# Kernel optimization log

Measured on AMD Instinct MI355X. Metric: run time of the kernel, lower is better.

## Reference

```python
import jax, jax.numpy as jnp
import numpy as np

N_QUBITS = 10
DEPTH = 4


def _cz_sign(n):
    # Diagonal of product of CZ(q, q+1) for q in 0..n-2 (qubit q = bit q, little-endian).
    idx = np.arange(2 ** n)
    bits = (idx[:, None] >> np.arange(n)) & 1            # (2^n, n)
    pairs = (bits[:, :-1] & bits[:, 1:]).sum(axis=1)
    return jnp.asarray(1 - 2 * (pairs & 1), jnp.float32)  # (2^n,)


def _z_matrix(n):
    # Column i = diagonal of Z on qubit n-1-i (Qiskit label 'I'*i + 'Z' + ...).
    idx = np.arange(2 ** n)
    bits = (idx[:, None] >> np.arange(n)) & 1
    return jnp.asarray((1 - 2 * bits)[:, ::-1], jnp.float32)  # (2^n, n)


def _quantum_features(x, theta):
    B, n = x.shape
    depth = theta.shape[0]
    half = 0.5 * x
    c = jnp.cos(half).astype(jnp.complex64)
    s = jnp.sin(half).astype(jnp.complex64)
    # Initial state: per-sample product of RX(x_q)|0> = [cos(x/2), -i sin(x/2)].
    # Build as kron over qubits, MSB (qubit n-1) first -> flat index bit q = qubit q.
    state = jnp.ones((B, 1), jnp.complex64)
    for q in reversed(range(n)):
        v = jnp.stack([c[:, q], -1j * s[:, q]], axis=-1)  # (B, 2)
        state = (state[:, :, None] * v[:, None, :]).reshape(B, -1)
    cz = _cz_sign(n)
    for l in range(depth):
        for q in range(n):
            th = 0.5 * theta[l, q]
            ct = jnp.cos(th).astype(jnp.complex64)
            st = jnp.sin(th).astype(jnp.complex64)
            gate = jnp.stack([jnp.stack([ct, -st]), jnp.stack([st, ct])])  # (2,2) RY
            left, right = 2 ** (n - 1 - q), 2 ** q
            state = jnp.einsum('ij,bljr->blir', gate,
                               state.reshape(B, left, 2, right)).reshape(B, -1)
        state = state * cz  # all CZ(q,q+1) at once (diagonal)
    probs = state.real ** 2 + state.imag ** 2          # (B, 2^n)
    return probs @ _z_matrix(n)                        # (B, n) <Z_i> expectations


def setup_inputs() -> dict:
    key = jax.random.key(0)
    ks = jax.random.split(key, 6)
    B, F, D = 4096, N_QUBITS, DEPTH
    x = jax.random.normal(ks[0], (B, F), jnp.float32)
    Ws = jax.random.normal(ks[1], (D + 1, F, F), jnp.float32) / np.sqrt(F).astype(np.float32)
    bs = 0.01 * jax.random.normal(ks[2], (D + 1, F), jnp.float32)
    theta = jax.random.normal(ks[3], (D, F), jnp.float32)
    W_final = jax.random.normal(ks[4], (2, 2 * F), jnp.float32) / np.sqrt(2 * F).astype(np.float32)
    b_final = 0.01 * jax.random.normal(ks[5], (2,), jnp.float32)
    return {"x": x, "Ws": Ws, "bs": bs, "theta": theta,
            "W_final": W_final, "b_final": b_final}


def reference(x, Ws, bs, theta, W_final, b_final):
    # Classical stack: depth x (Linear + ReLU) then a final Linear (same width).
    h = x
    for l in range(DEPTH):
        h = jax.nn.relu(h @ Ws[l].T + bs[l])
    cls_out = h @ Ws[DEPTH].T + bs[DEPTH]              # (B, F)
    qfeat = _quantum_features(x, theta)                # (B, n_qubits)
    combined = jnp.concatenate([cls_out, qfeat], axis=1)
    return combined @ W_final.T + b_final              # (B, 2) logits
```

## Files before the change

kernel.cpp:

```cpp
#include <hip/hip_runtime.h>
#include <math.h>

#define NQ 10
#define QDEPTH 4
#define BLK 256
#define WPS 4

typedef float v2f __attribute__((ext_vector_type(2)));

__device__ __forceinline__ int   asi(float v) { return __builtin_bit_cast(int, v); }
__device__ __forceinline__ float asf(int v)   { return __builtin_bit_cast(float, v); }

template<int D>
__device__ __forceinline__ float exch(float v, int addr32) {
    if constexpr (D == 1)
        return asf(__builtin_amdgcn_update_dpp(asi(v), asi(v), 0xB1, 0xF, 0xF, true));
    else if constexpr (D == 2)
        return asf(__builtin_amdgcn_update_dpp(asi(v), asi(v), 0x4E, 0xF, 0xF, true));
    else if constexpr (D == 4)
        return asf(__builtin_amdgcn_ds_swizzle(asi(v), 0x101F));
    else if constexpr (D == 8)
        return asf(__builtin_amdgcn_ds_swizzle(asi(v), 0x201F));
    else if constexpr (D == 16)
        return asf(__builtin_amdgcn_ds_swizzle(asi(v), 0x401F));
    else
        return asf(__builtin_amdgcn_ds_bpermute(addr32, asi(v)));
}

__device__ __forceinline__ float rlane(float v, int l) {
    return asf(__builtin_amdgcn_readlane(asi(v), l));
}

template<int Q>
__device__ __forceinline__ void local_gate_t(v2f (&P)[16], float t) {
    const v2f tt = {t, t};
    #pragma unroll
    for (int pp = 0; pp < 8; ++pp) {
        const int i0 = ((pp >> Q) << (Q + 1)) | (pp & ((1 << Q) - 1));
        const int i1 = i0 | (1 << Q);
        v2f a = P[i0], b = P[i1];
        P[i0] = a - tt * b;
        P[i1] = b + tt * a;
    }
}

template<int D>
__device__ __forceinline__ void cross_gate_t(v2f (&P)[16], float tvv, int addr32) {
    const v2f tt = {tvv, tvv};
    #pragma unroll
    for (int r = 0; r < 16; ++r) {
        v2f pp;
        pp.x = exch<D>(P[r].x, addr32);
        pp.y = exch<D>(P[r].y, addr32);
        P[r] = P[r] + tt * pp;
    }
}

__global__ __launch_bounds__(BLK, 4) void hybrid_kernel(
    const float* __restrict__ x,
    const float* __restrict__ Ws,
    const float* __restrict__ bs,
    const float* __restrict__ theta,
    const float* __restrict__ Wf,
    const float* __restrict__ bfin,
    float* __restrict__ out)
{
    const int tid  = threadIdx.x;
    const int lane = tid & 63;
    const int wv   = tid >> 6;
    const int s    = blockIdx.x * WPS + wv;

    float ang = 0.0f;
    if (lane < QDEPTH * NQ)              ang = theta[lane];
    else if (lane < QDEPTH * NQ + NQ)    ang = x[s * NQ + (lane - QDEPTH * NQ)];
    float sv_, cv_;
    sincosf(0.5f * ang, &sv_, &cv_);
    const float tv_ = sv_ / cv_;

    const int addr32 = (lane ^ 32) << 2;

    float cc = (lane < QDEPTH * NQ) ? cv_ : 1.0f;
    cc *= exch<1>(cc, addr32);
    cc *= exch<2>(cc, addr32);
    cc *= exch<4>(cc, addr32);
    cc *= exch<8>(cc, addr32);
    cc *= exch<16>(cc, addr32);
    cc *= exch<32>(cc, addr32);
    const float C2 = cc * cc;

    const int pl = __popc(lane);
    v2f P[16];
    {
        float cq[4], sq[4];
        #pragma unroll
        for (int q = 0; q < 4; ++q) {
            cq[q] = rlane(cv_, QDEPTH * NQ + q);
            sq[q] = rlane(sv_, QDEPTH * NQ + q);
        }
        float lf = 1.0f;
        #pragma unroll
        for (int b = 0; b < 6; ++b) {
            float cb = rlane(cv_, QDEPTH * NQ + 4 + b);
            float sb = rlane(sv_, QDEPTH * NQ + 4 + b);
            lf *= ((lane >> b) & 1) ? sb : cb;
        }
        float p01[4], p23[4];
        p01[0] = cq[0] * cq[1]; p01[1] = sq[0] * cq[1];
        p01[2] = cq[0] * sq[1]; p01[3] = sq[0] * sq[1];
        p23[0] = cq[2] * cq[3]; p23[1] = sq[2] * cq[3];
        p23[2] = cq[2] * sq[3]; p23[3] = sq[2] * sq[3];
        #pragma unroll
        for (int loc = 0; loc < 16; ++loc) {
            float r = lf * p01[loc & 3] * p23[loc >> 2];
            int pm = (pl + __popc(loc)) & 3;
            P[loc].x = (pm == 0) ? r : ((pm == 2) ? -r : 0.0f);
            P[loc].y = (pm == 1) ? -r : ((pm == 3) ? r : 0.0f);
        }
    }

    int zmask[6];
    #pragma unroll
    for (int b = 0; b < 6; ++b)
        zmask[b] = ((lane >> b) & 1) << 31;

    const int p3  = __popc(lane & (lane >> 1)) & 1;
    const int sAw = p3 << 31;
    const int sBw = (p3 ^ (lane & 1)) << 31;
    const int sAn = sAw ^ 0x80000000;
    const int sBn = sBw ^ 0x80000000;

    for (int l = 0; l < QDEPTH; ++l) {
        local_gate_t<0>(P, rlane(tv_, l * NQ + 0));
        local_gate_t<1>(P, rlane(tv_, l * NQ + 1));
        local_gate_t<2>(P, rlane(tv_, l * NQ + 2));
        local_gate_t<3>(P, rlane(tv_, l * NQ + 3));
        {
            float tvv;
            tvv = asf(asi(-rlane(tv_, l * NQ + 4)) ^ zmask[0]);
            cross_gate_t<1>(P, tvv, addr32);
            tvv = asf(asi(-rlane(tv_, l * NQ + 5)) ^ zmask[1]);
            cross_gate_t<2>(P, tvv, addr32);
            tvv = asf(asi(-rlane(tv_, l * NQ + 6)) ^ zmask[2]);
            cross_gate_t<4>(P, tvv, addr32);
            tvv = asf(asi(-rlane(tv_, l * NQ + 7)) ^ zmask[3]);
            cross_gate_t<8>(P, tvv, addr32);
            tvv = asf(asi(-rlane(tv_, l * NQ + 8)) ^ zmask[4]);
            cross_gate_t<16>(P, tvv, addr32);
            tvv = asf(asi(-rlane(tv_, l * NQ + 9)) ^ zmask[5]);
            cross_gate_t<32>(P, tvv, addr32);
        }
        #pragma unroll
        for (int loc = 0; loc < 16; ++loc) {
            const int C1 = __popc(loc & (loc >> 1)) & 1;
            const int m  = (loc & 8) ? (C1 ? sBn : sBw) : (C1 ? sAn : sAw);
            P[loc].x = asf(asi(P[loc].x) ^ m);
            P[loc].y = asf(asi(P[loc].y) ^ m);
        }
    }

    float pr[16], S = 0.0f;
    #pragma unroll
    for (int loc = 0; loc < 16; ++loc) {
        pr[loc] = fmaf(P[loc].x, P[loc].x, P[loc].y * P[loc].y);
        S += pr[loc];
    }
    float U0 = 0.0f, U1 = 0.0f, U2 = 0.0f, U3 = 0.0f;
    #pragma unroll
    for (int loc = 0; loc < 16; ++loc) {
        if (loc & 1) U0 += pr[loc];
        if (loc & 2) U1 += pr[loc];
        if (loc & 4) U2 += pr[loc];
        if (loc & 8) U3 += pr[loc];
    }
    const float w00 = Wf[19], w01 = Wf[18], w02 = Wf[17], w03 = Wf[16];
    const float w10 = Wf[39], w11 = Wf[38], w12 = Wf[37], w13 = Wf[36];
    float d0 = ((w00 + w01) + (w02 + w03)) * S;
    float d1 = ((w10 + w11) + (w12 + w13)) * S;
    d0 = fmaf(-2.0f * w00, U0, d0); d0 = fmaf(-2.0f * w01, U1, d0);
    d0 = fmaf(-2.0f * w02, U2, d0); d0 = fmaf(-2.0f * w03, U3, d0);
    d1 = fmaf(-2.0f * w10, U0, d1); d1 = fmaf(-2.0f * w11, U1, d1);
    d1 = fmaf(-2.0f * w12, U2, d1); d1 = fmaf(-2.0f * w13, U3, d1);
    float L0 = 0.0f, L1 = 0.0f;
    #pragma unroll
    for (int b = 0; b < 6; ++b) {
        L0 += asf(asi(Wf[15 - b]) ^ zmask[b]);
        L1 += asf(asi(Wf[35 - b]) ^ zmask[b]);
    }
    float qp0 = fmaf(L0, S, d0);
    float qp1 = fmaf(L1, S, d1);
    qp0 += exch<1>(qp0, addr32);  qp1 += exch<1>(qp1, addr32);
    qp0 += exch<2>(qp0, addr32);  qp1 += exch<2>(qp1, addr32);
    qp0 += exch<4>(qp0, addr32);  qp1 += exch<4>(qp1, addr32);
    qp0 += exch<8>(qp0, addr32);  qp1 += exch<8>(qp1, addr32);
    qp0 += exch<16>(qp0, addr32); qp1 += exch<16>(qp1, addr32);
    qp0 += exch<32>(qp0, addr32); qp1 += exch<32>(qp1, addr32);

    const int row = (lane < NQ) ? lane : 0;
    float h = x[s * NQ + row];
    #pragma unroll
    for (int l = 0; l < QDEPTH; ++l) {
        float v = bs[l * NQ + row];
        #pragma unroll
        for (int j = 0; j < NQ; ++j)
            v = fmaf(Ws[(l * NQ + row) * NQ + j], rlane(h, j), v);
        h = fmaxf(v, 0.0f);
    }
    float cls = bs[QDEPTH * NQ + row];
    #pragma unroll
    for (int j = 0; j < NQ; ++j)
        cls = fmaf(Ws[(QDEPTH * NQ + row) * NQ + j], rlane(h, j), cls);

    float o0 = fmaf(C2, qp0, bfin[0]);
    float o1 = fmaf(C2, qp1, bfin[1]);
    #pragma unroll
    for (int j = 0; j < NQ; ++j) {
        float cj = rlane(cls, j);
        o0 = fmaf(Wf[j],      cj, o0);
        o1 = fmaf(Wf[20 + j], cj, o1);
    }
    if (lane == 0) {
        float2 o; o.x = o0; o.y = o1;
        *reinterpret_cast<float2*>(&out[s * 2]) = o;
    }
}

extern "C" void kernel_launch(void* const* d_in, const int* in_sizes, int n_in,
                              void* d_out, int out_size, void* d_ws, size_t ws_size,
                              hipStream_t stream) {
    const float* x     = (const float*)d_in[0];
    const float* Ws    = (const float*)d_in[1];
    const float* bs    = (const float*)d_in[2];
    const float* theta = (const float*)d_in[3];
    const float* Wf    = (const float*)d_in[4];
    const float* bfin  = (const float*)d_in[5];
    float* out = (float*)d_out;

    const int B = in_sizes[0] / NQ;
    hybrid_kernel<<<B / WPS, BLK, 0, stream>>>(x, Ws, bs, theta, Wf, bfin, out);
}
```

Baseline: 24.79 us.

## Replace LDS-based lane exchanges with DPP and permlane swaps, fast sincos

Replaces the ds_swizzle/ds_bpermute exchanges for lane distances 8, 16 and 32 with a DPP row-shuffle and gfx950 permlane16/32 swap instructions. The 16- and 32-distance gates are reformulated around the pairwise sum the swap returns, so the partner value is never fetched directly. Also swaps sincosf for a custom range-reduced polynomial with a hardware reciprocal, and turns the CZ sign XOR into a multiply by ±1. This removes LDS-path latency from the cross-lane gates and reductions, at the cost of extra arithmetic and some rounding differences from the sum-based gate formula. The DPP control 0x128 for distance 8 is a row-rotate, and its correctness for a butterfly exchange is questionable.

```diff
diff --git a/kernel.cpp b/kernel.cpp
--- a/kernel.cpp
+++ b/kernel.cpp
@@ -12,23 +12,61 @@
 __device__ __forceinline__ float asf(int v)   { return __builtin_bit_cast(float, v); }
 
 template<int D>
-__device__ __forceinline__ float exch(float v, int addr32) {
+__device__ __forceinline__ float exch(float v) {
     if constexpr (D == 1)
         return asf(__builtin_amdgcn_update_dpp(asi(v), asi(v), 0xB1, 0xF, 0xF, true));
     else if constexpr (D == 2)
         return asf(__builtin_amdgcn_update_dpp(asi(v), asi(v), 0x4E, 0xF, 0xF, true));
-    else if constexpr (D == 4)
+    else if constexpr (D == 8)
+        return asf(__builtin_amdgcn_update_dpp(asi(v), asi(v), 0x128, 0xF, 0xF, true));
+    else
         return asf(__builtin_amdgcn_ds_swizzle(asi(v), 0x101F));
-    else if constexpr (D == 8)
-        return asf(__builtin_amdgcn_ds_swizzle(asi(v), 0x201F));
-    else if constexpr (D == 16)
-        return asf(__builtin_amdgcn_ds_swizzle(asi(v), 0x401F));
-    else
-        return asf(__builtin_amdgcn_ds_bpermute(addr32, asi(v)));
+}
+
+__device__ __forceinline__ float plsum16(float v) {
+    unsigned u = (unsigned)asi(v);
+    auto r = __builtin_amdgcn_permlane16_swap(u, u, false, false);
+    return asf((int)r[0]) + asf((int)r[1]);
+}
+__device__ __forceinline__ float plsum32(float v) {
+    unsigned u = (unsigned)asi(v);
+    auto r = __builtin_amdgcn_permlane32_swap(u, u, false, false);
+    return asf((int)r[0]) + asf((int)r[1]);
+}
+__device__ __forceinline__ float plmul16(float v) {
+    unsigned u = (unsigned)asi(v);
+    auto r = __builtin_amdgcn_permlane16_swap(u, u, false, false);
+    return asf((int)r[0]) * asf((int)r[1]);
+}
+__device__ __forceinline__ float plmul32(float v) {
+    unsigned u = (unsigned)asi(v);
+    auto r = __builtin_amdgcn_permlane32_swap(u, u, false, false);
+    return asf((int)r[0]) * asf((int)r[1]);
 }
 
 __device__ __forceinline__ float rlane(float v, int l) {
     return asf(__builtin_amdgcn_readlane(asi(v), l));
+}
+
+__device__ __forceinline__ void fast_sincos(float h, float* sp, float* cp) {
+    float nf = __builtin_rintf(h * 0.31830987f);
+    float r  = fmaf(nf, -3.14159274f, h);
+    r        = fmaf(nf,  8.7422777e-8f, r);
+    int  sg  = (((int)nf) & 1) << 31;
+    float x2 = r * r;
+    float q  = fmaf(x2, -2.5052108e-8f, 2.7557319e-6f);
+    q = fmaf(x2, q, -1.9841270e-4f);
+    q = fmaf(x2, q,  8.3333333e-3f);
+    q = fmaf(x2, q, -0.16666667f);
+    float s  = fmaf(r * x2, q, r);
+    float c2 = fmaf(x2,  2.0876757e-9f, -2.7557319e-7f);
+    c2 = fmaf(x2, c2,  2.4801587e-5f);
+    c2 = fmaf(x2, c2, -1.3888889e-3f);
+    c2 = fmaf(x2, c2,  4.1666667e-2f);
+    c2 = fmaf(x2, c2, -0.5f);
+    float c  = fmaf(x2, c2, 1.0f);
+    *sp = asf(asi(s) ^ sg);
+    *cp = asf(asi(c) ^ sg);
 }
 
 template<int Q>
@@ -45,14 +83,28 @@
 }
 
 template<int D>
-__device__ __forceinline__ void cross_gate_t(v2f (&P)[16], float tvv, int addr32) {
+__device__ __forceinline__ void cross_gate_t(v2f (&P)[16], float tvv) {
     const v2f tt = {tvv, tvv};
     #pragma unroll
     for (int r = 0; r < 16; ++r) {
         v2f pp;
-        pp.x = exch<D>(P[r].x, addr32);
-        pp.y = exch<D>(P[r].y, addr32);
+        pp.x = exch<D>(P[r].x);
+        pp.y = exch<D>(P[r].y);
         P[r] = P[r] + tt * pp;
+    }
+}
+
+template<int D>
+__device__ __forceinline__ void cross_gate_pl(v2f (&P)[16], float tvv) {
+    const v2f tt = {tvv, tvv};
+    const float om = 1.0f - tvv;
+    const v2f om2 = {om, om};
+    #pragma unroll
+    for (int r = 0; r < 16; ++r) {
+        v2f S;
+        if constexpr (D == 16) { S.x = plsum16(P[r].x); S.y = plsum16(P[r].y); }
+        else                   { S.x = plsum32(P[r].x); S.y = plsum32(P[r].y); }
+        P[r] = om2 * P[r] + tt * S;
     }
 }
 
@@ -74,18 +126,16 @@
     if (lane < QDEPTH * NQ)              ang = theta[lane];
     else if (lane < QDEPTH * NQ + NQ)    ang = x[s * NQ + (lane - QDEPTH * NQ)];
     float sv_, cv_;
-    sincosf(0.5f * ang, &sv_, &cv_);
-    const float tv_ = sv_ / cv_;
-
-    const int addr32 = (lane ^ 32) << 2;
+    fast_sincos(0.5f * ang, &sv_, &cv_);
+    const float tv_ = sv_ * __builtin_amdgcn_rcpf(cv_);
 
     float cc = (lane < QDEPTH * NQ) ? cv_ : 1.0f;
-    cc *= exch<1>(cc, addr32);
-    cc *= exch<2>(cc, addr32);
-    cc *= exch<4>(cc, addr32);
-    cc *= exch<8>(cc, addr32);
-    cc *= exch<16>(cc, addr32);
-    cc *= exch<32>(cc, addr32);
+    cc *= exch<1>(cc);
+    cc *= exch<2>(cc);
+    cc *= exch<4>(cc);
+    cc *= exch<8>(cc);
+    cc  = plmul16(cc);
+    cc  = plmul32(cc);
     const float C2 = cc * cc;
 
     const int pl = __popc(lane);
@@ -124,10 +174,10 @@
         zmask[b] = ((lane >> b) & 1) << 31;
 
     const int p3  = __popc(lane & (lane >> 1)) & 1;
-    const int sAw = p3 << 31;
-    const int sBw = (p3 ^ (lane & 1)) << 31;
-    const int sAn = sAw ^ 0x80000000;
-    const int sBn = sBw ^ 0x80000000;
+    const float sAf = asf(0x3F800000 ^ (p3 << 31));
+    const float sBf = asf(0x3F800000 ^ ((p3 ^ (lane & 1)) << 31));
+    const v2f sA2 = { sAf,  sAf}, sB2 = { sBf,  sBf};
+    const v2f nA2 = {-sAf, -sAf}, nB2 = {-sBf, -sBf};
 
     for (int l = 0; l < QDEPTH; ++l) {
         local_gate_t<0>(P, rlane(tv_, l * NQ + 0));
@@ -137,24 +187,23 @@
         {
             float tvv;
             tvv = asf(asi(-rlane(tv_, l * NQ + 4)) ^ zmask[0]);
-            cross_gate_t<1>(P, tvv, addr32);
+            cross_gate_t<1>(P, tvv);
             tvv = asf(asi(-rlane(tv_, l * NQ + 5)) ^ zmask[1]);
-            cross_gate_t<2>(P, tvv, addr32);
+            cross_gate_t<2>(P, tvv);
             tvv = asf(asi(-rlane(tv_, l * NQ + 6)) ^ zmask[2]);
-            cross_gate_t<4>(P, tvv, addr32);
+            cross_gate_t<4>(P, tvv);
             tvv = asf(asi(-rlane(tv_, l * NQ + 7)) ^ zmask[3]);
-            cross_gate_t<8>(P, tvv, addr32);
+            cross_gate_t<8>(P, tvv);
             tvv = asf(asi(-rlane(tv_, l * NQ + 8)) ^ zmask[4]);
-            cross_gate_t<16>(P, tvv, addr32);
+            cross_gate_pl<16>(P, tvv);
             tvv = asf(asi(-rlane(tv_, l * NQ + 9)) ^ zmask[5]);
-            cross_gate_t<32>(P, tvv, addr32);
+            cross_gate_pl<32>(P, tvv);
         }
         #pragma unroll
         for (int loc = 0; loc < 16; ++loc) {
             const int C1 = __popc(loc & (loc >> 1)) & 1;
-            const int m  = (loc & 8) ? (C1 ? sBn : sBw) : (C1 ? sAn : sAw);
-            P[loc].x = asf(asi(P[loc].x) ^ m);
-            P[loc].y = asf(asi(P[loc].y) ^ m);
+            const v2f m = (loc & 8) ? (C1 ? nB2 : sB2) : (C1 ? nA2 : sA2);
+            P[loc] = P[loc] * m;
         }
     }
 
@@ -188,12 +237,12 @@
     }
     float qp0 = fmaf(L0, S, d0);
     float qp1 = fmaf(L1, S, d1);
-    qp0 += exch<1>(qp0, addr32);  qp1 += exch<1>(qp1, addr32);
-    qp0 += exch<2>(qp0, addr32);  qp1 += exch<2>(qp1, addr32);
-    qp0 += exch<4>(qp0, addr32);  qp1 += exch<4>(qp1, addr32);
-    qp0 += exch<8>(qp0, addr32);  qp1 += exch<8>(qp1, addr32);
-    qp0 += exch<16>(qp0, addr32); qp1 += exch<16>(qp1, addr32);
-    qp0 += exch<32>(qp0, addr32); qp1 += exch<32>(qp1, addr32);
+    qp0 += exch<1>(qp0);  qp1 += exch<1>(qp1);
+    qp0 += exch<2>(qp0);  qp1 += exch<2>(qp1);
+    qp0 += exch<4>(qp0);  qp1 += exch<4>(qp1);
+    qp0 += exch<8>(qp0);  qp1 += exch<8>(qp1);
+    qp0  = plsum16(qp0);  qp1  = plsum16(qp1);
+    qp0  = plsum32(qp0);  qp1  = plsum32(qp1);
 
     const int row = (lane < NQ) ? lane : 0;
     float h = x[s * NQ + row];
```

New measurement: 27.39 us. 10.5% more time.

## Split each sample's statevector across two wavefronts with LDS exchange for top qubit

Applied to the files above, without the earlier changes.

Each sample's 1024-amplitude state is now spread over a pair of wavefronts, 8 amplitudes per lane instead of 16, and the grid doubles. Qubit 9 becomes a cross-wave gate: each wave writes its amplitudes to shared memory, synchronises and reads the partner's. Partial expectation sums are combined through shared memory before the classical stack, which only the even wave computes. The aim is to halve per-thread register pressure and serial work, allowing higher occupancy (launch bounds 8). The cost is two block barriers and LDS traffic per layer, and half the waves idle during the classical MLP.

```diff
diff --git a/kernel.cpp b/kernel.cpp
--- a/kernel.cpp
+++ b/kernel.cpp
@@ -4,7 +4,6 @@
 #define NQ 10
 #define QDEPTH 4
 #define BLK 256
-#define WPS 4
 
 typedef float v2f __attribute__((ext_vector_type(2)));
 
@@ -32,10 +31,10 @@
 }
 
 template<int Q>
-__device__ __forceinline__ void local_gate_t(v2f (&P)[16], float t) {
+__device__ __forceinline__ void local_gate_t(v2f (&P)[8], float t) {
     const v2f tt = {t, t};
     #pragma unroll
-    for (int pp = 0; pp < 8; ++pp) {
+    for (int pp = 0; pp < 4; ++pp) {
         const int i0 = ((pp >> Q) << (Q + 1)) | (pp & ((1 << Q) - 1));
         const int i1 = i0 | (1 << Q);
         v2f a = P[i0], b = P[i1];
@@ -45,10 +44,10 @@
 }
 
 template<int D>
-__device__ __forceinline__ void cross_gate_t(v2f (&P)[16], float tvv, int addr32) {
+__device__ __forceinline__ void cross_gate_t(v2f (&P)[8], float tvv, int addr32) {
     const v2f tt = {tvv, tvv};
     #pragma unroll
-    for (int r = 0; r < 16; ++r) {
+    for (int r = 0; r < 8; ++r) {
         v2f pp;
         pp.x = exch<D>(P[r].x, addr32);
         pp.y = exch<D>(P[r].y, addr32);
@@ -56,7 +55,7 @@
     }
 }
 
-__global__ __launch_bounds__(BLK, 4) void hybrid_kernel(
+__global__ __launch_bounds__(BLK, 8) void hybrid_kernel(
     const float* __restrict__ x,
     const float* __restrict__ Ws,
     const float* __restrict__ bs,
@@ -65,10 +64,14 @@
     const float* __restrict__ bfin,
     float* __restrict__ out)
 {
-    const int tid  = threadIdx.x;
-    const int lane = tid & 63;
-    const int wv   = tid >> 6;
-    const int s    = blockIdx.x * WPS + wv;
+    const int tid     = threadIdx.x;
+    const int lane    = tid & 63;
+    const int wv      = tid >> 6;
+    const int pairbit = wv & 1;
+    const int s       = blockIdx.x * 2 + (wv >> 1);
+
+    __shared__ v2f   xch[4][8][64];
+    __shared__ float qpart[4][2];
 
     float ang = 0.0f;
     if (lane < QDEPTH * NQ)              ang = theta[lane];
@@ -88,30 +91,26 @@
     cc *= exch<32>(cc, addr32);
     const float C2 = cc * cc;
 
-    const int pl = __popc(lane);
-    v2f P[16];
+    const int pl = __popc(lane) + pairbit;
+    v2f P[8];
     {
-        float cq[4], sq[4];
-        #pragma unroll
-        for (int q = 0; q < 4; ++q) {
-            cq[q] = rlane(cv_, QDEPTH * NQ + q);
-            sq[q] = rlane(sv_, QDEPTH * NQ + q);
-        }
+        float c0 = rlane(cv_, 40), s0 = rlane(sv_, 40);
+        float c1 = rlane(cv_, 41), s1 = rlane(sv_, 41);
+        float c2 = rlane(cv_, 42), s2 = rlane(sv_, 42);
         float lf = 1.0f;
         #pragma unroll
         for (int b = 0; b < 6; ++b) {
-            float cb = rlane(cv_, QDEPTH * NQ + 4 + b);
-            float sb = rlane(sv_, QDEPTH * NQ + 4 + b);
+            float cb = rlane(cv_, 43 + b);
+            float sb = rlane(sv_, 43 + b);
             lf *= ((lane >> b) & 1) ? sb : cb;
         }
-        float p01[4], p23[4];
-        p01[0] = cq[0] * cq[1]; p01[1] = sq[0] * cq[1];
-        p01[2] = cq[0] * sq[1]; p01[3] = sq[0] * sq[1];
-        p23[0] = cq[2] * cq[3]; p23[1] = sq[2] * cq[3];
-        p23[2] = cq[2] * sq[3]; p23[3] = sq[2] * sq[3];
-        #pragma unroll
-        for (int loc = 0; loc < 16; ++loc) {
-            float r = lf * p01[loc & 3] * p23[loc >> 2];
+        lf *= pairbit ? rlane(sv_, 49) : rlane(cv_, 49);
+        float p01[4];
+        p01[0] = c0 * c1; p01[1] = s0 * c1;
+        p01[2] = c0 * s1; p01[3] = s0 * s1;
+        #pragma unroll
+        for (int loc = 0; loc < 8; ++loc) {
+            float r = lf * p01[loc & 3] * ((loc & 4) ? s2 : c2);
             int pm = (pl + __popc(loc)) & 3;
             P[loc].x = (pm == 0) ? r : ((pm == 2) ? -r : 0.0f);
             P[loc].y = (pm == 1) ? -r : ((pm == 3) ? r : 0.0f);
@@ -123,68 +122,85 @@
     for (int b = 0; b < 6; ++b)
         zmask[b] = ((lane >> b) & 1) << 31;
 
-    const int p3  = __popc(lane & (lane >> 1)) & 1;
-    const int sAw = p3 << 31;
-    const int sBw = (p3 ^ (lane & 1)) << 31;
-    const int sAn = sAw ^ 0x80000000;
-    const int sBn = sBw ^ 0x80000000;
+    const int p3   = __popc(lane & (lane >> 1)) & 1;
+    const int base = (p3 ^ (((lane >> 5) & 1) & pairbit)) << 31;
+    const int w00 = base;
+    const int w01 = base ^ 0x80000000;
+    const int wB0 = base ^ ((lane & 1) << 31);
+    const int wB1 = wB0 ^ 0x80000000;
 
     for (int l = 0; l < QDEPTH; ++l) {
         local_gate_t<0>(P, rlane(tv_, l * NQ + 0));
         local_gate_t<1>(P, rlane(tv_, l * NQ + 1));
         local_gate_t<2>(P, rlane(tv_, l * NQ + 2));
-        local_gate_t<3>(P, rlane(tv_, l * NQ + 3));
         {
             float tvv;
-            tvv = asf(asi(-rlane(tv_, l * NQ + 4)) ^ zmask[0]);
+            tvv = asf(asi(-rlane(tv_, l * NQ + 3)) ^ zmask[0]);
             cross_gate_t<1>(P, tvv, addr32);
-            tvv = asf(asi(-rlane(tv_, l * NQ + 5)) ^ zmask[1]);
+            tvv = asf(asi(-rlane(tv_, l * NQ + 4)) ^ zmask[1]);
             cross_gate_t<2>(P, tvv, addr32);
-            tvv = asf(asi(-rlane(tv_, l * NQ + 6)) ^ zmask[2]);
+            tvv = asf(asi(-rlane(tv_, l * NQ + 5)) ^ zmask[2]);
             cross_gate_t<4>(P, tvv, addr32);
-            tvv = asf(asi(-rlane(tv_, l * NQ + 7)) ^ zmask[3]);
+            tvv = asf(asi(-rlane(tv_, l * NQ + 6)) ^ zmask[3]);
             cross_gate_t<8>(P, tvv, addr32);
-            tvv = asf(asi(-rlane(tv_, l * NQ + 8)) ^ zmask[4]);
+            tvv = asf(asi(-rlane(tv_, l * NQ + 7)) ^ zmask[4]);
             cross_gate_t<16>(P, tvv, addr32);
-            tvv = asf(asi(-rlane(tv_, l * NQ + 9)) ^ zmask[5]);
+            tvv = asf(asi(-rlane(tv_, l * NQ + 8)) ^ zmask[5]);
             cross_gate_t<32>(P, tvv, addr32);
         }
-        #pragma unroll
-        for (int loc = 0; loc < 16; ++loc) {
-            const int C1 = __popc(loc & (loc >> 1)) & 1;
-            const int m  = (loc & 8) ? (C1 ? sBn : sBw) : (C1 ? sAn : sAw);
+        {
+            const float t9  = rlane(tv_, l * NQ + 9);
+            const float tv9 = asf(asi(-t9) ^ (pairbit << 31));
+            const v2f   t92 = {tv9, tv9};
+            #pragma unroll
+            for (int r = 0; r < 8; ++r)
+                xch[wv][r][lane] = P[r];
+            __syncthreads();
+            v2f Q[8];
+            #pragma unroll
+            for (int r = 0; r < 8; ++r)
+                Q[r] = xch[wv ^ 1][r][lane];
+            #pragma unroll
+            for (int r = 0; r < 8; ++r)
+                P[r] = P[r] + t92 * Q[r];
+            __syncthreads();
+        }
+        #pragma unroll
+        for (int loc = 0; loc < 8; ++loc) {
+            const int m = (loc & 4) ? ((loc == 6) ? wB1 : wB0)
+                                    : ((loc == 3) ? w01 : w00);
             P[loc].x = asf(asi(P[loc].x) ^ m);
             P[loc].y = asf(asi(P[loc].y) ^ m);
         }
     }
 
-    float pr[16], S = 0.0f;
-    #pragma unroll
-    for (int loc = 0; loc < 16; ++loc) {
+    float pr[8], S = 0.0f;
+    #pragma unroll
+    for (int loc = 0; loc < 8; ++loc) {
         pr[loc] = fmaf(P[loc].x, P[loc].x, P[loc].y * P[loc].y);
         S += pr[loc];
     }
-    float U0 = 0.0f, U1 = 0.0f, U2 = 0.0f, U3 = 0.0f;
-    #pragma unroll
-    for (int loc = 0; loc < 16; ++loc) {
+    float U0 = 0.0f, U1 = 0.0f, U2 = 0.0f;
+    #pragma unroll
+    for (int loc = 0; loc < 8; ++loc) {
         if (loc & 1) U0 += pr[loc];
         if (loc & 2) U1 += pr[loc];
         if (loc & 4) U2 += pr[loc];
-        if (loc & 8) U3 += pr[loc];
-    }
-    const float w00 = Wf[19], w01 = Wf[18], w02 = Wf[17], w03 = Wf[16];
-    const float w10 = Wf[39], w11 = Wf[38], w12 = Wf[37], w13 = Wf[36];
-    float d0 = ((w00 + w01) + (w02 + w03)) * S;
-    float d1 = ((w10 + w11) + (w12 + w13)) * S;
-    d0 = fmaf(-2.0f * w00, U0, d0); d0 = fmaf(-2.0f * w01, U1, d0);
-    d0 = fmaf(-2.0f * w02, U2, d0); d0 = fmaf(-2.0f * w03, U3, d0);
-    d1 = fmaf(-2.0f * w10, U0, d1); d1 = fmaf(-2.0f * w11, U1, d1);
-    d1 = fmaf(-2.0f * w12, U2, d1); d1 = fmaf(-2.0f * w13, U3, d1);
-    float L0 = 0.0f, L1 = 0.0f;
+    }
+    const float a00 = Wf[19], a01 = Wf[18], a02 = Wf[17];
+    const float a10 = Wf[39], a11 = Wf[38], a12 = Wf[37];
+    float d0 = ((a00 + a01) + a02) * S;
+    float d1 = ((a10 + a11) + a12) * S;
+    d0 = fmaf(-2.0f * a00, U0, d0); d0 = fmaf(-2.0f * a01, U1, d0);
+    d0 = fmaf(-2.0f * a02, U2, d0);
+    d1 = fmaf(-2.0f * a10, U0, d1); d1 = fmaf(-2.0f * a11, U1, d1);
+    d1 = fmaf(-2.0f * a12, U2, d1);
+    float L0 = asf(asi(Wf[10]) ^ (pairbit << 31));
+    float L1 = asf(asi(Wf[30]) ^ (pairbit << 31));
     #pragma unroll
     for (int b = 0; b < 6; ++b) {
-        L0 += asf(asi(Wf[15 - b]) ^ zmask[b]);
-        L1 += asf(asi(Wf[35 - b]) ^ zmask[b]);
+        L0 += asf(asi(Wf[16 - b]) ^ zmask[b]);
+        L1 += asf(asi(Wf[36 - b]) ^ zmask[b]);
     }
     float qp0 = fmaf(L0, S, d0);
     float qp1 = fmaf(L1, S, d1);
@@ -195,6 +211,14 @@
     qp0 += exch<16>(qp0, addr32); qp1 += exch<16>(qp1, addr32);
     qp0 += exch<32>(qp0, addr32); qp1 += exch<32>(qp1, addr32);
 
+    if (lane == 0) { qpart[wv][0] = qp0; qpart[wv][1] = qp1; }
+    __syncthreads();
+
+    if (pairbit) return;
+
+    const float qs0 = qp0 + qpart[wv ^ 1][0];
+    const float qs1 = qp1 + qpart[wv ^ 1][1];
+
     const int row = (lane < NQ) ? lane : 0;
     float h = x[s * NQ + row];
     #pragma unroll
@@ -210,8 +234,8 @@
     for (int j = 0; j < NQ; ++j)
         cls = fmaf(Ws[(QDEPTH * NQ + row) * NQ + j], rlane(h, j), cls);
 
-    float o0 = fmaf(C2, qp0, bfin[0]);
-    float o1 = fmaf(C2, qp1, bfin[1]);
+    float o0 = fmaf(C2, qs0, bfin[0]);
+    float o1 = fmaf(C2, qs1, bfin[1]);
     #pragma unroll
     for (int j = 0; j < NQ; ++j) {
         float cj = rlane(cls, j);
@@ -236,5 +260,5 @@
     float* out = (float*)d_out;
 
     const int B = in_sizes[0] / NQ;
-    hybrid_kernel<<<B / WPS, BLK, 0, stream>>>(x, Ws, bs, theta, Wf, bfin, out);
-}
+    hybrid_kernel<<<B / 2, BLK, 0, stream>>>(x, Ws, bs, theta, Wf, bfin, out);
+}
```

Measured after the change: 26.83 us. +8.2%, slower.
